# Kernel tuning notes

Measured on AMD Instinct MI355X. Metric: run time of the kernel, lower is better.

Reference implementation:

```python
import jax, jax.numpy as jnp
import numpy as np

E = 1024      # embed_dim (== embed_dim_)
NH = 8        # num_heads
HD = E // NH  # head_dim
BS1 = 2048
BS2 = 2048
EPS = 1e-5


def _layernorm(x, g, b):
    m = jnp.mean(x, axis=-1, keepdims=True)
    v = jnp.mean(jnp.square(x - m), axis=-1, keepdims=True)
    return (x - m) * jax.lax.rsqrt(v + EPS) * g + b


def setup_inputs() -> dict:
    key = jax.random.key(0)
    ks = jax.random.split(key, 16)
    s = 1.0 / np.sqrt(E)
    s4 = 1.0 / np.sqrt(4 * E)
    inp = {
        "x1": jax.random.normal(ks[0], (BS1, E), jnp.float32),
        "x2": jax.random.normal(ks[1], (BS2, E), jnp.float32),
        "Wq": jax.random.uniform(ks[2], (E, E), jnp.float32, -s, s),
        "bq": jax.random.uniform(ks[3], (E,), jnp.float32, -s, s),
        "Wk": jax.random.uniform(ks[4], (E, E), jnp.float32, -s, s),
        "bk": jax.random.uniform(ks[5], (E,), jnp.float32, -s, s),
        "Wv": jax.random.uniform(ks[6], (E, E), jnp.float32, -s, s),
        "bv": jax.random.uniform(ks[7], (E,), jnp.float32, -s, s),
        "Wo": jax.random.uniform(ks[8], (E, E), jnp.float32, -s, s),
        "bo": jax.random.uniform(ks[9], (E,), jnp.float32, -s, s),
        "W1": jax.random.uniform(ks[10], (4 * E, E), jnp.float32, -s, s),
        "b1": jax.random.uniform(ks[11], (4 * E,), jnp.float32, -s, s),
        "W2": jax.random.uniform(ks[12], (E, 4 * E), jnp.float32, -s4, s4),
        "b2": jax.random.uniform(ks[13], (E,), jnp.float32, -s4, s4),
        "g1": jnp.ones((E,), jnp.float32),
        "be1": jnp.zeros((E,), jnp.float32),
        "g2": jnp.ones((E,), jnp.float32),
        "be2": jnp.zeros((E,), jnp.float32),
    }
    return inp


def reference(x1, x2, Wq, bq, Wk, bk, Wv, bv, Wo, bo, W1, b1, W2, b2, g1, be1, g2, be2):
    scale = HD ** -0.5
    # Projections; attention runs over the batch axis (n=bs1, m=bs2)
    q = (x1 @ Wq.T + bq).reshape(BS1, NH, HD)   # [n,h,d]
    k = (x2 @ Wk.T + bk).reshape(BS2, NH, HD)   # [m,h,d]
    v = (x2 @ Wv.T + bv).reshape(BS2, NH, HD)   # [m,h,d]
    scores = jnp.einsum('nhd,mhd->nmh', q, k) * scale  # [n,m,h]
    # NOTE: faithful to source: softmax over the HEADS axis (dim=-1)
    probs = jax.nn.softmax(scores, axis=-1)
    # dropout is identity in eval mode
    attn = jnp.einsum('nmh,mhd->nhd', probs, v).reshape(BS1, E)
    attn = attn @ Wo.T + bo
    h = _layernorm(x1 + attn, g1, be1)
    ffn = jax.nn.relu(h @ W1.T + b1) @ W2.T + b2
    return _layernorm(h + ffn, g2, be2)
```

## Files before the change

### kernel.cpp

```cpp
#include <hip/hip_runtime.h>

#define BS 2048
#define EMB 1024
#define NHEAD 8
#define HDIM 128

typedef unsigned short u16;
typedef __attribute__((ext_vector_type(8))) short bf16x8;
typedef __attribute__((ext_vector_type(4))) float f32x4;

__device__ __forceinline__ u16 f32_bf16(float f) {
  unsigned u = __float_as_uint(f);
  u += 0x7fffu + ((u >> 16) & 1u);
  return (u16)(u >> 16);
}
__device__ __forceinline__ float bf2f(u16 x) {
  return __uint_as_float((unsigned)x << 16);
}

__device__ __forceinline__ void gld_lds16(const void* g, void* l) {
  __builtin_amdgcn_global_load_lds(
      (const __attribute__((address_space(1))) void*)g,
      (__attribute__((address_space(3))) void*)l, 16, 0, 0);
}

struct CvtArgs { const float* src[8]; };
__global__ __launch_bounds__(256) void cvt_all(CvtArgs a, u16* __restrict__ dst) {
  long i = (long)blockIdx.x * 256 + threadIdx.x;
  int seg = (int)(i >> 18);
  const float* src; long b;
  if (seg < 2)       { src = a.src[0]; b = 0; }
  else if (seg < 4)  { src = a.src[1]; b = 2L << 18; }
  else if (seg == 4) { src = a.src[2]; b = 4L << 18; }
  else if (seg == 5) { src = a.src[3]; b = 5L << 18; }
  else if (seg == 6) { src = a.src[4]; b = 6L << 18; }
  else if (seg == 7) { src = a.src[5]; b = 7L << 18; }
  else if (seg < 12) { src = a.src[6]; b = 8L << 18; }
  else               { src = a.src[7]; b = 12L << 18; }
  float4 v = ((const float4*)src)[i - b];
  ushort4 o;
  o.x = f32_bf16(v.x); o.y = f32_bf16(v.y); o.z = f32_bf16(v.z); o.w = f32_bf16(v.w);
  ((ushort4*)dst)[i] = o;
}

__device__ __forceinline__ void gemm_core(
    const u16* __restrict__ A, const u16* __restrict__ B, void* __restrict__ Cp,
    const float* __restrict__ bias, int K, int lda, int ldb, int ldc,
    long cbase, int mode, int relu, int m0, int n0) {
  __shared__ __align__(16) u16 As[128 * 32];
  __shared__ __align__(16) u16 Bs[128 * 32];
  const int t = threadIdx.x;
  const int lane = t & 63, l15 = lane & 15, quad = lane >> 4;
  const int wv = t >> 6, wr = wv & 1, wc = wv >> 1;
  const int wbase = t & ~63;

  f32x4 acc[4][4];
#pragma unroll
  for (int r = 0; r < 4; ++r)
#pragma unroll
    for (int c = 0; c < 4; ++c) acc[r][c] = (f32x4){0.f, 0.f, 0.f, 0.f};

  for (int k0 = 0; k0 < K; k0 += 32) {
#pragma unroll
    for (int i = 0; i < 2; ++i) {
      int s = i * 256 + t;
      gld_lds16(A + (long)(m0 + (s >> 2)) * lda + k0 + (s & 3) * 8,
                As + (i * 256 + wbase) * 8);
    }
#pragma unroll
    for (int i = 0; i < 2; ++i) {
      int s = i * 256 + t;
      gld_lds16(B + (long)(n0 + (s >> 2)) * ldb + k0 + (s & 3) * 8,
                Bs + (i * 256 + wbase) * 8);
    }
    __syncthreads();
    bf16x8 fa[4], fb[4];
#pragma unroll
    for (int r = 0; r < 4; ++r)
      fa[r] = *(const bf16x8*)&As[(wr * 64 + r * 16 + l15) * 32 + quad * 8];
#pragma unroll
    for (int c = 0; c < 4; ++c)
      fb[c] = *(const bf16x8*)&Bs[(wc * 64 + c * 16 + l15) * 32 + quad * 8];
#pragma unroll
    for (int r = 0; r < 4; ++r)
#pragma unroll
      for (int c = 0; c < 4; ++c)
        acc[r][c] = __builtin_amdgcn_mfma_f32_16x16x32_bf16(fa[r], fb[c], acc[r][c], 0, 0, 0);
    __syncthreads();
  }

#pragma unroll
  for (int r = 0; r < 4; ++r)
#pragma unroll
    for (int c = 0; c < 4; ++c) {
      const int m = m0 + wr * 64 + r * 16 + quad * 4;
      const int n = n0 + wc * 64 + c * 16 + l15;
      const float bv = bias ? bias[n] : 0.f;
      f32x4 v = acc[r][c];
      if (mode == 2) {
        ushort4 o;
        o.x = f32_bf16(v[0] + bv);
        o.y = f32_bf16(v[1] + bv);
        o.z = f32_bf16(v[2] + bv);
        o.w = f32_bf16(v[3] + bv);
        *(ushort4*)((u16*)Cp + cbase + (long)n * ldc + m) = o;
      } else {
#pragma unroll
        for (int i = 0; i < 4; ++i) {
          float x = v[i] + bv;
          if (relu) x = fmaxf(x, 0.f);
          if (mode == 0)
            ((float*)Cp)[cbase + (long)(m + i) * ldc + n] = x;
          else
            ((u16*)Cp)[cbase + (long)(m + i) * ldc + n] = f32_bf16(x);
        }
      }
    }
}

__global__ __launch_bounds__(256) void gemm_bt_k(
    const u16* __restrict__ A, const u16* __restrict__ B, void* __restrict__ C,
    const float* __restrict__ bias, int K, int lda, int ldb, int ldc,
    long aOffZ, long bOffZ, long cOffZ, int mode, int relu) {
  gemm_core(A + (long)blockIdx.z * aOffZ, B + (long)blockIdx.z * bOffZ, C, bias,
            K, lda, ldb, ldc, (long)blockIdx.z * cOffZ, mode, relu,
            blockIdx.y * 128, blockIdx.x * 128);
}

__global__ __launch_bounds__(256) void qkv_kernel(
    const u16* __restrict__ x1b, const u16* __restrict__ x2b,
    const u16* __restrict__ Wqb, const u16* __restrict__ Wkb, const u16* __restrict__ Wvb,
    const float* __restrict__ bq, const float* __restrict__ bk, const float* __restrict__ bv,
    u16* __restrict__ Qb, u16* __restrict__ Kb, u16* __restrict__ Vt) {
  const int z = blockIdx.z;
  const u16* A = (z == 0) ? x1b : x2b;
  const u16* B = (z == 0) ? Wqb : (z == 1) ? Wkb : Wvb;
  void* C = (z == 0) ? (void*)Qb : (z == 1) ? (void*)Kb : (void*)Vt;
  const float* bias = (z == 0) ? bq : (z == 1) ? bk : bv;
  const int mode = (z == 2) ? 2 : 1;
  const int ldc = (z == 2) ? 2048 : 1024;
  gemm_core(A, B, C, bias, 1024, 1024, 1024, ldc, 0, mode, 0,
            blockIdx.y * 128, blockIdx.x * 128);
}

__global__ __launch_bounds__(256) void pv_kernel(
    const u16* __restrict__ P, const u16* __restrict__ Vt,
    u16* p0, u16* p1, u16* p2, u16* p3) {
  const int h = blockIdx.z >> 2, ks = blockIdx.z & 3;
  u16* parts = (ks == 0) ? p0 : (ks == 1) ? p1 : (ks == 2) ? p2 : p3;
  const u16* A = P + (long)h * BS * BS + ks * 512;
  const u16* B = Vt + (long)h * HDIM * 2048 + ks * 512;
  gemm_core(A, B, parts, nullptr, 512, 2048, 2048, 1024, (long)h * HDIM, 1, 0,
            blockIdx.y * 128, 0);
}

__global__ __launch_bounds__(256) void reduce4p_bf16(
    const u16* __restrict__ p0, const u16* __restrict__ p1,
    const u16* __restrict__ p2, const u16* __restrict__ p3, u16* __restrict__ out) {
  long i = (long)blockIdx.x * 256 + threadIdx.x;
  ushort4 a = ((const ushort4*)p0)[i];
  ushort4 b = ((const ushort4*)p1)[i];
  ushort4 c = ((const ushort4*)p2)[i];
  ushort4 d = ((const ushort4*)p3)[i];
  ushort4 o;
  o.x = f32_bf16(bf2f(a.x) + bf2f(b.x) + bf2f(c.x) + bf2f(d.x));
  o.y = f32_bf16(bf2f(a.y) + bf2f(b.y) + bf2f(c.y) + bf2f(d.y));
  o.z = f32_bf16(bf2f(a.z) + bf2f(b.z) + bf2f(c.z) + bf2f(d.z));
  o.w = f32_bf16(bf2f(a.w) + bf2f(b.w) + bf2f(c.w) + bf2f(d.w));
  ((ushort4*)out)[i] = o;
}

__global__ __launch_bounds__(256) void scores_softmax(
    const u16* __restrict__ Q, const u16* __restrict__ Km, u16* __restrict__ P) {
  __shared__ __align__(16) u16 Qs[2][4096];
  __shared__ __align__(16) u16 Ks[2][16384];
  const int t = threadIdx.x;
  const int lane = t & 63, l15 = lane & 15, quad = lane >> 4;
  const int wv = t >> 6, wbase = t & ~63;
  const int n0 = blockIdx.y * 32, m0 = blockIdx.x * 128;

  auto stage = [&](int h, int b) {
#pragma unroll
    for (int i = 0; i < 2; ++i) {
      int s = i * 256 + t;
      gld_lds16(Q + (long)(n0 + ((s >> 2) & 31)) * EMB + h * HDIM + (s >> 7) * 32 + (s & 3) * 8,
                &Qs[b][(i * 256 + wbase) * 8]);
    }
#pragma unroll
    for (int i = 0; i < 8; ++i) {
      int s = i * 256 + t;
      gld_lds16(Km + (long)(m0 + ((s >> 2) & 127)) * EMB + h * HDIM + (s >> 9) * 32 + (s & 3) * 8,
                &Ks[b][(i * 256 + wbase) * 8]);
    }
  };

  f32x4 acc[8][2][2];
#pragma unroll
  for (int h = 0; h < 8; ++h)
#pragma unroll
    for (int r = 0; r < 2; ++r)
#pragma unroll
      for (int c = 0; c < 2; ++c) acc[h][r][c] = (f32x4){0.f, 0.f, 0.f, 0.f};

  stage(0, 0);
#pragma unroll
  for (int h = 0; h < 8; ++h) {
    __syncthreads();
    if (h < 7) stage(h + 1, (h + 1) & 1);
    const u16* qb = Qs[h & 1];
    const u16* kb = Ks[h & 1];
#pragma unroll
    for (int kk = 0; kk < 4; ++kk) {
      bf16x8 fa[2], fb[2];
#pragma unroll
      for (int r = 0; r < 2; ++r)
        fa[r] = *(const bf16x8*)&qb[kk * 1024 + (r * 16 + l15) * 32 + quad * 8];
#pragma unroll
      for (int c = 0; c < 2; ++c)
        fb[c] = *(const bf16x8*)&kb[kk * 4096 + (wv * 32 + c * 16 + l15) * 32 + quad * 8];
#pragma unroll
      for (int r = 0; r < 2; ++r)
#pragma unroll
        for (int c = 0; c < 2; ++c)
          acc[h][r][c] = __builtin_amdgcn_mfma_f32_16x16x32_bf16(fa[r], fb[c], acc[h][r][c], 0, 0, 0);
    }
  }

  const float scale = 0.08838834764831845f;
#pragma unroll
  for (int r = 0; r < 2; ++r)
#pragma unroll
    for (int c = 0; c < 2; ++c)
#pragma unroll
      for (int i = 0; i < 4; ++i) {
        float mx = acc[0][r][c][i];
#pragma unroll
        for (int h = 1; h < 8; ++h) mx = fmaxf(mx, acc[h][r][c][i]);
        float sum = 0.f;
#pragma unroll
        for (int h = 0; h < 8; ++h) {
          float e = __expf((acc[h][r][c][i] - mx) * scale);
          acc[h][r][c][i] = e;
          sum += e;
        }
        float inv = 1.f / sum;
#pragma unroll
        for (int h = 0; h < 8; ++h) acc[h][r][c][i] *= inv;
      }

#pragma unroll
  for (int h = 0; h < 8; ++h) {
    u16* ph = P + (long)h * BS * BS;
#pragma unroll
    for (int r = 0; r < 2; ++r)
#pragma unroll
      for (int c = 0; c < 2; ++c)
#pragma unroll
        for (int i = 0; i < 4; ++i)
          ph[(long)(n0 + r * 16 + quad * 4 + i) * BS + m0 + wv * 32 + c * 16 + l15] =
              f32_bf16(acc[h][r][c][i]);
  }
}

__global__ __launch_bounds__(256) void ln_residual_p4(
    const float* __restrict__ x,
    const u16* __restrict__ p0, const u16* __restrict__ p1,
    const u16* __restrict__ p2, const u16* __restrict__ p3,
    const float* __restrict__ colb, const float* __restrict__ g, const float* __restrict__ b,
    float* __restrict__ out32, u16* __restrict__ out16) {
  const int row = blockIdx.x, t = threadIdx.x;
  const long base = (long)row * EMB;
  float4 v = ((const float4*)(x + base))[t];
  ushort4 a0 = ((const ushort4*)(p0 + base))[t];
  ushort4 a1 = ((const ushort4*)(p1 + base))[t];
  ushort4 a2 = ((const ushort4*)(p2 + base))[t];
  ushort4 a3 = ((const ushort4*)(p3 + base))[t];
  float4 cb = ((const float4*)colb)[t];
  v.x += bf2f(a0.x) + bf2f(a1.x) + bf2f(a2.x) + bf2f(a3.x) + cb.x;
  v.y += bf2f(a0.y) + bf2f(a1.y) + bf2f(a2.y) + bf2f(a3.y) + cb.y;
  v.z += bf2f(a0.z) + bf2f(a1.z) + bf2f(a2.z) + bf2f(a3.z) + cb.z;
  v.w += bf2f(a0.w) + bf2f(a1.w) + bf2f(a2.w) + bf2f(a3.w) + cb.w;
  float s = v.x + v.y + v.z + v.w;
  float q = v.x * v.x + v.y * v.y + v.z * v.z + v.w * v.w;
#pragma unroll
  for (int off = 32; off > 0; off >>= 1) {
    s += __shfl_xor(s, off);
    q += __shfl_xor(q, off);
  }
  __shared__ float red[8];
  const int wv = t >> 6, lane = t & 63;
  if (lane == 0) { red[wv] = s; red[4 + wv] = q; }
  __syncthreads();
  s = red[0] + red[1] + red[2] + red[3];
  q = red[4] + red[5] + red[6] + red[7];
  const float mean = s * (1.f / EMB);
  const float var = q * (1.f / EMB) - mean * mean;
  const float rstd = rsqrtf(var + 1e-5f);
  float4 gg = ((const float4*)g)[t];
  float4 bb = ((const float4*)b)[t];
  float4 o;
  o.x = (v.x - mean) * rstd * gg.x + bb.x;
  o.y = (v.y - mean) * rstd * gg.y + bb.y;
  o.z = (v.z - mean) * rstd * gg.z + bb.z;
  o.w = (v.w - mean) * rstd * gg.w + bb.w;
  ((float4*)(out32 + base))[t] = o;
  if (out16) {
    ushort4 ho;
    ho.x = f32_bf16(o.x); ho.y = f32_bf16(o.y); ho.z = f32_bf16(o.z); ho.w = f32_bf16(o.w);
    ((ushort4*)(out16 + base))[t] = ho;
  }
}

extern "C" void kernel_launch(void* const* d_in, const int* in_sizes, int n_in,
                              void* d_out, int out_size, void* d_ws, size_t ws_size,
                              hipStream_t stream) {
  const float* x1 = (const float*)d_in[0];
  const float* x2 = (const float*)d_in[1];
  const float* Wq = (const float*)d_in[2];
  const float* bq = (const float*)d_in[3];
  const float* Wk = (const float*)d_in[4];
  const float* bk = (const float*)d_in[5];
  const float* Wv = (const float*)d_in[6];
  const float* bv = (const float*)d_in[7];
  const float* Wo = (const float*)d_in[8];
  const float* bo = (const float*)d_in[9];
  const float* W1 = (const float*)d_in[10];
  const float* b1 = (const float*)d_in[11];
  const float* W2 = (const float*)d_in[12];
  const float* b2 = (const float*)d_in[13];
  const float* g1 = (const float*)d_in[14];
  const float* be1 = (const float*)d_in[15];
  const float* g2 = (const float*)d_in[16];
  const float* be2 = (const float*)d_in[17];

  char* ws = (char*)d_ws;
  const size_t MB = 1ull << 20;
  u16* x1b = (u16*)(ws + 0 * MB);
  u16* x2b = (u16*)(ws + 4 * MB);
  u16* Wqb = (u16*)(ws + 8 * MB);
  u16* Wkb = (u16*)(ws + 10 * MB);
  u16* Wvb = (u16*)(ws + 12 * MB);
  u16* Wob = (u16*)(ws + 14 * MB);
  u16* W1b = (u16*)(ws + 16 * MB);
  u16* W2b = (u16*)(ws + 24 * MB);
  u16* Qb  = (u16*)(ws + 32 * MB);
  u16* Kb  = (u16*)(ws + 36 * MB);
  u16* Vtb = (u16*)(ws + 40 * MB);
  u16* attnb = (u16*)(ws + 44 * MB);
  u16* P   = (u16*)(ws + 48 * MB);
  u16* woP[4] = {(u16*)(ws + 48 * MB), (u16*)(ws + 52 * MB),
                 (u16*)(ws + 56 * MB), (u16*)(ws + 60 * MB)};
  float* h32  = (float*)(ws + 64 * MB);
  u16*  h16   = (u16*)(ws + 72 * MB);
  u16*  ffn1b = (u16*)(ws + 76 * MB);
  u16* f2P[4] = {(u16*)(ws + 92 * MB), (u16*)(ws + 96 * MB),
                 (u16*)(ws + 100 * MB), (u16*)(ws + 104 * MB)};

  CvtArgs ca;
  ca.src[0] = x1; ca.src[1] = x2; ca.src[2] = Wq; ca.src[3] = Wk;
  ca.src[4] = Wv; ca.src[5] = Wo; ca.src[6] = W1; ca.src[7] = W2;
  cvt_all<<<16384, 256, 0, stream>>>(ca, (u16*)ws);

  qkv_kernel<<<dim3(8, 16, 3), 256, 0, stream>>>(x1b, x2b, Wqb, Wkb, Wvb, bq, bk, bv, Qb, Kb, Vtb);

  scores_softmax<<<dim3(16, 64), 256, 0, stream>>>(Qb, Kb, P);

  pv_kernel<<<dim3(1, 16, 32), 256, 0, stream>>>(P, Vtb, x1b, x2b, Qb, Kb);

  reduce4p_bf16<<<2048, 256, 0, stream>>>(x1b, x2b, Qb, Kb, attnb);

  gemm_bt_k<<<dim3(8, 16, 4), 256, 0, stream>>>(attnb, Wob, woP[0], nullptr,
                                                256, 1024, 1024, 1024,
                                                256, 256, (long)BS * 1024, 1, 0);

  ln_residual_p4<<<2048, 256, 0, stream>>>(x1, woP[0], woP[1], woP[2], woP[3],
                                           bo, g1, be1, h32, h16);

  gemm_bt_k<<<dim3(32, 16, 1), 256, 0, stream>>>(h16, W1b, ffn1b, b1,
                                                 1024, 1024, 1024, 4096,
                                                 0, 0, 0, 1, 1);

  gemm_bt_k<<<dim3(8, 16, 4), 256, 0, stream>>>(ffn1b, W2b, f2P[0], nullptr,
                                                1024, 4096, 4096, 1024,
                                                1024, 1024, (long)BS * 1024, 1, 0);

  ln_residual_p4<<<2048, 256, 0, stream>>>(h32, f2P[0], f2P[1], f2P[2], f2P[3],
                                           b2, g2, be2, (float*)d_out, nullptr);
}
```

Before: 339.2 us.

## Fuse scores, head-softmax and PV into one attention kernel

```diff
diff --git a/kernel.cpp b/kernel.cpp
--- a/kernel.cpp
+++ b/kernel.cpp
@@ -143,15 +143,133 @@
             blockIdx.y * 128, blockIdx.x * 128);
 }
 
-__global__ __launch_bounds__(256) void pv_kernel(
-    const u16* __restrict__ P, const u16* __restrict__ Vt,
-    u16* p0, u16* p1, u16* p2, u16* p3) {
-  const int h = blockIdx.z >> 2, ks = blockIdx.z & 3;
-  u16* parts = (ks == 0) ? p0 : (ks == 1) ? p1 : (ks == 2) ? p2 : p3;
-  const u16* A = P + (long)h * BS * BS + ks * 512;
-  const u16* B = Vt + (long)h * HDIM * 2048 + ks * 512;
-  gemm_core(A, B, parts, nullptr, 512, 2048, 2048, 1024, (long)h * HDIM, 1, 0,
-            blockIdx.y * 128, 0);
+__global__ __launch_bounds__(256, 2) void fused_attn3(
+    const u16* __restrict__ Qg, const u16* __restrict__ Kg,
+    const u16* __restrict__ Vt, u16* __restrict__ parts) {
+  __shared__ __align__(16) u16 Qs[2048 * 8];
+  __shared__ __align__(16) u16 KV[2048 * 8];
+  __shared__ __align__(16) u16 Ps[256 * 8];
+  const int t = threadIdx.x;
+  const int lane = t & 63, l15 = lane & 15, quad = lane >> 4;
+  const int wv = t >> 6, wbase = t & ~63;
+  const int chunk = blockIdx.x;
+  const int n0 = blockIdx.y * 16;
+
+#pragma unroll
+  for (int i = 0; i < 8; ++i) {
+    int c = i * 256 + t;
+    int n = c >> 7;
+    int kc = (c & 127) ^ (n & 15);
+    gld_lds16(Qg + (long)(n0 + n) * EMB + kc * 8, Qs + (i * 256 + wbase) * 8);
+  }
+
+  f32x4 O[8][2];
+#pragma unroll
+  for (int h = 0; h < 8; ++h)
+#pragma unroll
+    for (int d = 0; d < 2; ++d) O[h][d] = (f32x4){0.f, 0.f, 0.f, 0.f};
+
+  const float scale = 0.08838834764831845f;
+
+  for (int g = 0; g < 4; ++g) {
+    const int m0 = chunk * 512 + g * 128;
+
+    f32x4 acc[8][2];
+#pragma unroll
+    for (int h = 0; h < 8; ++h)
+#pragma unroll
+      for (int tt = 0; tt < 2; ++tt) acc[h][tt] = (f32x4){0.f, 0.f, 0.f, 0.f};
+
+#pragma unroll 1
+    for (int h = 0; h < 8; ++h) {
+      __syncthreads();
+#pragma unroll
+      for (int i = 0; i < 8; ++i) {
+        int c = i * 256 + t;
+        int row = c >> 4;
+        int kc = (c & 15) ^ (row & 15);
+        gld_lds16(Kg + (long)(m0 + row) * EMB + h * HDIM + kc * 8,
+                  KV + (i * 256 + wbase) * 8);
+      }
+      __syncthreads();
+#pragma unroll
+      for (int kk = 0; kk < 4; ++kk) {
+        bf16x8 fb = *(const bf16x8*)&Qs[(l15 * 128 + ((h * 16 + kk * 4 + quad) ^ l15)) * 8];
+#pragma unroll
+        for (int tt = 0; tt < 2; ++tt) {
+          int row = wv * 32 + tt * 16 + l15;
+          bf16x8 fa = *(const bf16x8*)&KV[(row * 16 + ((kk * 4 + quad) ^ l15)) * 8];
+          acc[h][tt] = __builtin_amdgcn_mfma_f32_16x16x32_bf16(fa, fb, acc[h][tt], 0, 0, 0);
+        }
+      }
+    }
+
+#pragma unroll
+    for (int tt = 0; tt < 2; ++tt)
+#pragma unroll
+      for (int i = 0; i < 4; ++i) {
+        float mx = acc[0][tt][i];
+#pragma unroll
+        for (int h = 1; h < 8; ++h) mx = fmaxf(mx, acc[h][tt][i]);
+        float sum = 0.f;
+#pragma unroll
+        for (int h = 0; h < 8; ++h) {
+          float e = __expf((acc[h][tt][i] - mx) * scale);
+          acc[h][tt][i] = e;
+          sum += e;
+        }
+        float inv = 1.f / sum;
+#pragma unroll
+        for (int h = 0; h < 8; ++h) acc[h][tt][i] *= inv;
+      }
+
+#pragma unroll 1
+    for (int h = 0; h < 8; ++h) {
+      __syncthreads();
+#pragma unroll
+      for (int tt = 0; tt < 2; ++tt) {
+        int mc = wv * 4 + tt * 2 + (quad >> 1);
+        ushort4 o4;
+        o4.x = f32_bf16(acc[h][tt][0]);
+        o4.y = f32_bf16(acc[h][tt][1]);
+        o4.z = f32_bf16(acc[h][tt][2]);
+        o4.w = f32_bf16(acc[h][tt][3]);
+        *(ushort4*)&Ps[(l15 * 16 + (mc ^ l15)) * 8 + (quad & 1) * 4] = o4;
+      }
+#pragma unroll
+      for (int i = 0; i < 8; ++i) {
+        int c = i * 256 + t;
+        int row = c >> 4;
+        int kc = (c & 15) ^ (row & 15);
+        gld_lds16(Vt + (long)(h * HDIM + row) * 2048 + m0 + kc * 8,
+                  KV + (i * 256 + wbase) * 8);
+      }
+      __syncthreads();
+#pragma unroll
+      for (int kk = 0; kk < 4; ++kk) {
+        bf16x8 pb = *(const bf16x8*)&Ps[(l15 * 16 + ((kk * 4 + quad) ^ l15)) * 8];
+#pragma unroll
+        for (int dt = 0; dt < 2; ++dt) {
+          int row = wv * 32 + dt * 16 + l15;
+          bf16x8 va = *(const bf16x8*)&KV[(row * 16 + ((kk * 4 + quad) ^ l15)) * 8];
+          O[h][dt] = __builtin_amdgcn_mfma_f32_16x16x32_bf16(va, pb, O[h][dt], 0, 0, 0);
+        }
+      }
+    }
+  }
+
+  u16* pbase = parts + (long)chunk * BS * EMB + (long)(n0 + l15) * EMB;
+#pragma unroll
+  for (int h = 0; h < 8; ++h)
+#pragma unroll
+    for (int dt = 0; dt < 2; ++dt) {
+      ushort4 o4;
+      o4.x = f32_bf16(O[h][dt][0]);
+      o4.y = f32_bf16(O[h][dt][1]);
+      o4.z = f32_bf16(O[h][dt][2]);
+      o4.w = f32_bf16(O[h][dt][3]);
+      *(ushort4*)&pbase[h * HDIM + wv * 32 + dt * 16 + quad * 4] = o4;
+    }
 }
 
 __global__ __launch_bounds__(256) void reduce4p_bf16(
@@ -168,98 +286,6 @@
   o.z = f32_bf16(bf2f(a.z) + bf2f(b.z) + bf2f(c.z) + bf2f(d.z));
   o.w = f32_bf16(bf2f(a.w) + bf2f(b.w) + bf2f(c.w) + bf2f(d.w));
   ((ushort4*)out)[i] = o;
-}
-
-__global__ __launch_bounds__(256) void scores_softmax(
-    const u16* __restrict__ Q, const u16* __restrict__ Km, u16* __restrict__ P) {
-  __shared__ __align__(16) u16 Qs[2][4096];
-  __shared__ __align__(16) u16 Ks[2][16384];
-  const int t = threadIdx.x;
-  const int lane = t & 63, l15 = lane & 15, quad = lane >> 4;
-  const int wv = t >> 6, wbase = t & ~63;
-  const int n0 = blockIdx.y * 32, m0 = blockIdx.x * 128;
-
-  auto stage = [&](int h, int b) {
-#pragma unroll
-    for (int i = 0; i < 2; ++i) {
-      int s = i * 256 + t;
-      gld_lds16(Q + (long)(n0 + ((s >> 2) & 31)) * EMB + h * HDIM + (s >> 7) * 32 + (s & 3) * 8,
-                &Qs[b][(i * 256 + wbase) * 8]);
-    }
-#pragma unroll
-    for (int i = 0; i < 8; ++i) {
-      int s = i * 256 + t;
-      gld_lds16(Km + (long)(m0 + ((s >> 2) & 127)) * EMB + h * HDIM + (s >> 9) * 32 + (s & 3) * 8,
-                &Ks[b][(i * 256 + wbase) * 8]);
-    }
-  };
-
-  f32x4 acc[8][2][2];
-#pragma unroll
-  for (int h = 0; h < 8; ++h)
-#pragma unroll
-    for (int r = 0; r < 2; ++r)
-#pragma unroll
-      for (int c = 0; c < 2; ++c) acc[h][r][c] = (f32x4){0.f, 0.f, 0.f, 0.f};
-
-  stage(0, 0);
-#pragma unroll
-  for (int h = 0; h < 8; ++h) {
-    __syncthreads();
-    if (h < 7) stage(h + 1, (h + 1) & 1);
-    const u16* qb = Qs[h & 1];
-    const u16* kb = Ks[h & 1];
-#pragma unroll
-    for (int kk = 0; kk < 4; ++kk) {
-      bf16x8 fa[2], fb[2];
-#pragma unroll
-      for (int r = 0; r < 2; ++r)
-        fa[r] = *(const bf16x8*)&qb[kk * 1024 + (r * 16 + l15) * 32 + quad * 8];
-#pragma unroll
-      for (int c = 0; c < 2; ++c)
-        fb[c] = *(const bf16x8*)&kb[kk * 4096 + (wv * 32 + c * 16 + l15) * 32 + quad * 8];
-#pragma unroll
-      for (int r = 0; r < 2; ++r)
-#pragma unroll
-        for (int c = 0; c < 2; ++c)
-          acc[h][r][c] = __builtin_amdgcn_mfma_f32_16x16x32_bf16(fa[r], fb[c], acc[h][r][c], 0, 0, 0);
-    }
-  }
-
-  const float scale = 0.08838834764831845f;
-#pragma unroll
-  for (int r = 0; r < 2; ++r)
-#pragma unroll
-    for (int c = 0; c < 2; ++c)
-#pragma unroll
-      for (int i = 0; i < 4; ++i) {
-        float mx = acc[0][r][c][i];
-#pragma unroll
-        for (int h = 1; h < 8; ++h) mx = fmaxf(mx, acc[h][r][c][i]);
-        float sum = 0.f;
-#pragma unroll
-        for (int h = 0; h < 8; ++h) {
-          float e = __expf((acc[h][r][c][i] - mx) * scale);
-          acc[h][r][c][i] = e;
-          sum += e;
-        }
-        float inv = 1.f / sum;
-#pragma unroll
-        for (int h = 0; h < 8; ++h) acc[h][r][c][i] *= inv;
-      }
-
-#pragma unroll
-  for (int h = 0; h < 8; ++h) {
-    u16* ph = P + (long)h * BS * BS;
-#pragma unroll
-    for (int r = 0; r < 2; ++r)
-#pragma unroll
-      for (int c = 0; c < 2; ++c)
-#pragma unroll
-        for (int i = 0; i < 4; ++i)
-          ph[(long)(n0 + r * 16 + quad * 4 + i) * BS + m0 + wv * 32 + c * 16 + l15] =
-              f32_bf16(acc[h][r][c][i]);
-  }
 }
 
 __global__ __launch_bounds__(256) void ln_residual_p4(
@@ -347,7 +373,7 @@
   u16* Kb  = (u16*)(ws + 36 * MB);
   u16* Vtb = (u16*)(ws + 40 * MB);
   u16* attnb = (u16*)(ws + 44 * MB);
-  u16* P   = (u16*)(ws + 48 * MB);
+  u16* Oparts = (u16*)(ws + 48 * MB);
   u16* woP[4] = {(u16*)(ws + 48 * MB), (u16*)(ws + 52 * MB),
                  (u16*)(ws + 56 * MB), (u16*)(ws + 60 * MB)};
   float* h32  = (float*)(ws + 64 * MB);
@@ -363,11 +389,11 @@
 
   qkv_kernel<<<dim3(8, 16, 3), 256, 0, stream>>>(x1b, x2b, Wqb, Wkb, Wvb, bq, bk, bv, Qb, Kb, Vtb);
 
-  scores_softmax<<<dim3(16, 64), 256, 0, stream>>>(Qb, Kb, P);
-
-  pv_kernel<<<dim3(1, 16, 32), 256, 0, stream>>>(P, Vtb, x1b, x2b, Qb, Kb);
-
-  reduce4p_bf16<<<2048, 256, 0, stream>>>(x1b, x2b, Qb, Kb, attnb);
+  fused_attn3<<<dim3(4, 128), 256, 0, stream>>>(Qb, Kb, Vtb, Oparts);
+
+  const long S = (long)BS * EMB;
+  reduce4p_bf16<<<2048, 256, 0, stream>>>(Oparts, Oparts + S, Oparts + 2 * S,
+                                          Oparts + 3 * S, attnb);
 
   gemm_bt_k<<<dim3(8, 16, 4), 256, 0, stream>>>(attnb, Wob, woP[0], nullptr,
                                                 256, 1024, 1024, 1024,
```

After: 537.6 us. 1.58x slower.
